# Optimization experiments

Measured on AMD Instinct MI355X. Metric: run time of the kernel, lower is better.

Reference implementation:

```python
import jax, jax.numpy as jnp
import numpy as np

D_MODEL = 1024
N_HEADS = 16
D_FF = 4096
EPS = 1e-6


def _linear_params(key, d_in, d_out):
    kw, kb = jax.random.split(key)
    bound = 1.0 / np.sqrt(d_in)
    W = jax.random.uniform(kw, (d_out, d_in), minval=-bound, maxval=bound, dtype=jnp.float32)
    b = jax.random.uniform(kb, (d_out,), minval=-bound, maxval=bound, dtype=jnp.float32)
    return W, b


def setup_inputs() -> dict:
    key = jax.random.key(0)
    keys = jax.random.split(key, 8)
    x = jax.random.normal(keys[0], (4, 2048, D_MODEL), dtype=jnp.float32)
    mask = jnp.ones((4, 1, 1, 2048), dtype=jnp.bool_)
    Wq, bq = _linear_params(keys[1], D_MODEL, D_MODEL)
    Wk, bk = _linear_params(keys[2], D_MODEL, D_MODEL)
    Wv, bv = _linear_params(keys[3], D_MODEL, D_MODEL)
    Wo, bo = _linear_params(keys[4], D_MODEL, D_MODEL)
    W1, b1 = _linear_params(keys[5], D_MODEL, D_FF)
    W2, b2 = _linear_params(keys[6], D_FF, D_MODEL)
    ln1_g = jnp.ones((D_MODEL,), jnp.float32); ln1_b = jnp.zeros((D_MODEL,), jnp.float32)
    ln2_g = jnp.ones((D_MODEL,), jnp.float32); ln2_b = jnp.zeros((D_MODEL,), jnp.float32)
    return {"x": x, "mask": mask,
            "Wq": Wq, "bq": bq, "Wk": Wk, "bk": bk, "Wv": Wv, "bv": bv,
            "Wo": Wo, "bo": bo, "W1": W1, "b1": b1, "W2": W2, "b2": b2,
            "ln1_g": ln1_g, "ln1_b": ln1_b, "ln2_g": ln2_g, "ln2_b": ln2_b}


def _layernorm(x, g, b):
    # torch LayerNorm here uses unbiased std and divides by (std + eps)
    mean = jnp.mean(x, axis=-1, keepdims=True)
    std = jnp.std(x, axis=-1, keepdims=True, ddof=1)
    return g * (x - mean) / (std + EPS) + b


def _gelu_tanh(x):
    c = np.sqrt(2.0 / np.pi).astype(np.float32)
    return 0.5 * x * (1.0 + jnp.tanh(c * (x + 0.044715 * x * x * x)))


def _mha(xn, mask, Wq, bq, Wk, bk, Wv, bv, Wo, bo):
    B, S, D = xn.shape
    d_k = D // N_HEADS
    def proj(W, b):
        y = jnp.einsum('bsd,ed->bse', xn, W) + b
        return y.reshape(B, S, N_HEADS, d_k).transpose(0, 2, 1, 3)  # [B,h,S,d_k]
    q, k, v = proj(Wq, bq), proj(Wk, bk), proj(Wv, bv)
    scores = jnp.einsum('bhqd,bhkd->bhqk', q, k) / np.float32(np.sqrt(d_k))
    scores = jnp.where(mask, scores, jnp.float32(-1e9))
    p = jax.nn.softmax(scores, axis=-1)
    o = jnp.einsum('bhqk,bhkd->bhqd', p, v)
    o = o.transpose(0, 2, 1, 3).reshape(B, S, D)
    return jnp.einsum('bsd,ed->bse', o, Wo) + bo


def reference(x, mask, Wq, bq, Wk, bk, Wv, bv, Wo, bo, W1, b1, W2, b2,
              ln1_g, ln1_b, ln2_g, ln2_b):
    xn = _layernorm(x, ln1_g, ln1_b)
    y = x + _mha(xn, mask, Wq, bq, Wk, bk, Wv, bv, Wo, bo)
    yn = _layernorm(y, ln2_g, ln2_b)
    h = _gelu_tanh(jnp.einsum('bsd,fd->bsf', yn, W1) + b1)
    z = y + (jnp.einsum('bsf,df->bsd', h, W2) + b2)
    return z
```

## Files before the change

### kernel.cpp

```cpp
#include <hip/hip_runtime.h>

typedef __bf16 bf16;
typedef __bf16 bfx4 __attribute__((ext_vector_type(4)));
typedef __bf16 bfx8 __attribute__((ext_vector_type(8)));
typedef float  fx4  __attribute__((ext_vector_type(4)));

#define NTOK 8192
#define DM   1024
#define DFF  4096
#define SEQ  2048
#define NH   16
#define DK   64

#define OFF_WQKV 0ull
#define OFF_WO   (OFF_WQKV + 3072ull*1024*2)
#define OFF_W1   (OFF_WO   + 1024ull*1024*2)
#define OFF_W2   (OFF_W1   + 4096ull*1024*2)
#define OFF_BQKV (OFF_W2   + 4096ull*1024*2)
#define OFF_XN   (OFF_BQKV + 3072ull*4)
#define OFF_QKV  (OFF_XN   + 8192ull*1024*2)
#define OFF_ATTN (OFF_QKV  + 8192ull*3072*2)
#define OFF_Y    (OFF_ATTN + 8192ull*1024*2)
#define OFF_VT   OFF_Y
#define OFF_H    OFF_XN
#define OFF_YN   OFF_ATTN

__device__ __forceinline__ void gload16(const void* g, void* l) {
  __builtin_amdgcn_global_load_lds(
      (__attribute__((address_space(1))) void*)(g),
      (__attribute__((address_space(3))) void*)(l), 16, 0, 0);
}

__device__ __forceinline__ float gelu_tanh(float x) {
  float u = 0.7978845608028654f * (x + 0.044715f * x * x * x);
  float t = 1.f - 2.f / (__expf(2.f * u) + 1.f);
  return 0.5f * x * (1.f + t);
}

__global__ __launch_bounds__(256) void cast_all(const float* __restrict__ Wq,
                                                const float* __restrict__ Wk,
                                                const float* __restrict__ Wv,
                                                const float* __restrict__ Wo,
                                                const float* __restrict__ W1,
                                                const float* __restrict__ W2,
                                                bf16* __restrict__ dst) {
  const int bid = blockIdx.x;
  const int g = bid >> 9;
  const int j = ((bid & 511) << 11) + threadIdx.x * 8;
  const float* s;
  if (g == 0) s = Wq;
  else if (g == 1) s = Wk;
  else if (g == 2) s = Wv;
  else if (g == 3) s = Wo;
  else if (g < 8) s = W1 + (size_t)(g - 4) * 1048576;
  else s = W2 + (size_t)(g - 8) * 1048576;
  const float4 a = *(const float4*)(s + j);
  const float4 c = *(const float4*)(s + j + 4);
  bfx8 o;
  o[0] = (bf16)a.x; o[1] = (bf16)a.y; o[2] = (bf16)a.z; o[3] = (bf16)a.w;
  o[4] = (bf16)c.x; o[5] = (bf16)c.y; o[6] = (bf16)c.z; o[7] = (bf16)c.w;
  *(bfx8*)(dst + (size_t)g * 1048576 + j) = o;
}

__global__ void biask(const float* __restrict__ bq, const float* __restrict__ bk,
                      const float* __restrict__ bv, float* __restrict__ o) {
  const int i = blockIdx.x * 1024 + threadIdx.x;
  const float* s = blockIdx.x == 0 ? bq : (blockIdx.x == 1 ? bk : bv);
  o[i] = s[threadIdx.x];
}

__global__ __launch_bounds__(256) void ln_kernel(const float* __restrict__ x,
                                                 const float* __restrict__ g,
                                                 const float* __restrict__ b,
                                                 bf16* __restrict__ out) {
  const int row = blockIdx.x;
  const int c = threadIdx.x * 4;
  const float4 v = *(const float4*)&x[(size_t)row * DM + c];
  float s1 = v.x + v.y + v.z + v.w;
  float s2 = v.x * v.x + v.y * v.y + v.z * v.z + v.w * v.w;
  #pragma unroll
  for (int o = 32; o; o >>= 1) { s1 += __shfl_xor(s1, o); s2 += __shfl_xor(s2, o); }
  __shared__ float red[8];
  const int wid = threadIdx.x >> 6;
  if ((threadIdx.x & 63) == 0) { red[wid] = s1; red[4 + wid] = s2; }
  __syncthreads();
  s1 = red[0] + red[1] + red[2] + red[3];
  s2 = red[4] + red[5] + red[6] + red[7];
  const float mean = s1 * (1.f / (float)DM);
  const float var = (s2 - (float)DM * mean * mean) * (1.f / (float)(DM - 1));
  const float inv = 1.f / (sqrtf(fmaxf(var, 0.f)) + 1e-6f);
  bfx4 o;
  o[0] = (bf16)(g[c + 0] * (v.x - mean) * inv + b[c + 0]);
  o[1] = (bf16)(g[c + 1] * (v.y - mean) * inv + b[c + 1]);
  o[2] = (bf16)(g[c + 2] * (v.z - mean) * inv + b[c + 2]);
  o[3] = (bf16)(g[c + 3] * (v.w - mean) * inv + b[c + 3]);
  *(bfx4*)&out[(size_t)row * DM + c] = o;
}

template <int EPI, int VSPLIT>
__global__ __launch_bounds__(256) void gemmdp(const bf16* __restrict__ A,
                                              const bf16* __restrict__ B,
                                              const float* __restrict__ bias,
                                              const float* __restrict__ resid,
                                              bf16* __restrict__ vt,
                                              void* __restrict__ outp,
                                              int M, int N, int K) {
  __shared__ char lds[65536];
  const int tid = threadIdx.x;
  const int lane = tid & 63, w = tid >> 6;
  const int l15 = lane & 15, lhi = lane >> 4;
  const int wm = w >> 1, wn = w & 1;

  const int nwg = gridDim.x * gridDim.y;
  int bid = blockIdx.y * gridDim.x + blockIdx.x;
  bid = (bid & 7) * (nwg >> 3) + (bid >> 3);
  const int m0 = (bid % gridDim.x) * 128;
  const int n0 = (bid / gridDim.x) * 128;
  const size_t str = (size_t)K * 2;

  const int r_s = tid >> 3;
  const int c2  = (tid & 7) * 16;
  const int csw = c2 ^ ((r_s & 7) << 4);
  const char* ap = (const char*)A + (size_t)(m0 + r_s) * str + csw;
  const char* bp = (const char*)B + (size_t)(n0 + r_s) * str + csw;

  auto stage = [&](int buf) {
    char* dst = lds + buf * 32768 + tid * 16;
    #pragma unroll
    for (int s = 0; s < 4; ++s)
      gload16(ap + (size_t)(s * 32) * str, dst + s * 4096);
    #pragma unroll
    for (int s = 0; s < 4; ++s)
      gload16(bp + (size_t)(s * 32) * str, dst + 16384 + s * 4096);
    ap += 128; bp += 128;
  };

  fx4 acc[4][4] = {};
  const int asw = (l15 & 7) << 4;
  const int nK = K >> 6;

  stage(0);

  #pragma unroll 1
  for (int t = 0; t < nK; ++t) {
    asm volatile("s_waitcnt vmcnt(0)" ::: "memory");
    __builtin_amdgcn_s_barrier();
    asm volatile("" ::: "memory");
    if (t + 1 < nK) stage((t + 1) & 1);

    const char* Ab = lds + (t & 1) * 32768;
    const char* Bb = Ab + 16384;
    #pragma unroll
    for (int kk = 0; kk < 2; ++kk) {
      bfx8 af[4], bv[4];
      #pragma unroll
      for (int i = 0; i < 4; ++i)
        af[i] = *(const bfx8*)(Ab + (wm * 64 + i * 16 + l15) * 128 +
                               ((kk * 64 + lhi * 16) ^ asw));
      #pragma unroll
      for (int j = 0; j < 4; ++j)
        bv[j] = *(const bfx8*)(Bb + (wn * 64 + j * 16 + l15) * 128 +
                               ((kk * 64 + lhi * 16) ^ asw));
      __builtin_amdgcn_s_setprio(1);
      #pragma unroll
      for (int i = 0; i < 4; ++i)
        #pragma unroll
        for (int j = 0; j < 4; ++j)
          acc[i][j] = __builtin_amdgcn_mfma_f32_16x16x32_bf16(af[i], bv[j], acc[i][j], 0, 0, 0);
      __builtin_amdgcn_s_setprio(0);
    }
  }

  const int rb = m0 + wm * 64 + lhi * 4;
  const int cb = n0 + wn * 64 + l15;
  #pragma unroll
  for (int j = 0; j < 4; ++j) {
    const int c = cb + j * 16;
    const float bv = bias[c];
    if (VSPLIT && c >= 2048) {
      const int hd = c - 2048;
      #pragma unroll
      for (int i = 0; i < 4; ++i) {
        const int tok = rb + i * 16;
        const int bb = tok >> 11;
        bfx4 o4;
        #pragma unroll
        for (int e = 0; e < 4; ++e) o4[e] = (bf16)(acc[i][j][e] + bv);
        *(bfx4*)&vt[((size_t)(bb * 1024 + hd)) * SEQ + (tok & 2047)] = o4;
      }
    } else {
      #pragma unroll
      for (int i = 0; i < 4; ++i) {
        #pragma unroll
        for (int e = 0; e < 4; ++e) {
          const size_t idx = (size_t)(rb + i * 16 + e) * N + c;
          float v = acc[i][j][e] + bv;
          if constexpr (EPI == 1) v = gelu_tanh(v);
          if constexpr (EPI == 2) {
            ((float*)outp)[idx] = v + resid[idx];
          } else {
            ((bf16*)outp)[idx] = (bf16)v;
          }
        }
      }
    }
  }
}

__global__ __launch_bounds__(256, 4) void attn_kernel(const bf16* __restrict__ QKV,
                                                      const bf16* __restrict__ VT,
                                                      bf16* __restrict__ O) {
  __shared__ bf16 lds[2][2][4096];
  const int tid = threadIdx.x;
  const int lane = tid & 63, w = tid >> 6;
  const int l15 = lane & 15, lhi = lane >> 4;
  int id = blockIdx.x;
  id = (id & 7) * 128 + (id >> 3);
  const int q0 = (id & 15) * 128;
  const int h = (id >> 4) & 15;
  const int b = id >> 8;
  const size_t tokbase = (size_t)b * SEQ;

  const int lin0 = w * 1024 + lane * 16;
  const int lin1 = lin0 + 4096;
  const int row0 = lin0 >> 7, row1 = lin1 >> 7;
  const int cs0 = (lin0 & 127) ^ ((row0 & 7) << 4);
  const int cs1 = (lin1 & 127) ^ ((row1 & 7) << 4);
  const char* kp0 = (const char*)QKV + ((tokbase + row0) * 3072 + 1024 + h * 64) * 2 + cs0;
  const char* kp1 = (const char*)QKV + ((tokbase + row1) * 3072 + 1024 + h * 64) * 2 + cs1;
  const char* vbase = (const char*)(VT + (size_t)((b * NH + h) * 64) * SEQ);
  const char* vp0 = vbase + (size_t)row0 * (SEQ * 2) + cs0;
  const char* vp1 = vbase + (size_t)row1 * (SEQ * 2) + cs1;
  char* const ldsb = (char*)&lds[0][0][0];
  int dofs = 0;
  const long KADV = 64l * 3072 * 2;
  const long VADV = 64l * 2;

  auto stage = [&]() {
    gload16(kp0, ldsb + dofs + lin0);
    gload16(kp1, ldsb + dofs + lin1);
    gload16(vp0, ldsb + dofs + 8192 + lin0);
    gload16(vp1, ldsb + dofs + 8192 + lin1);
    kp0 += KADV; kp1 += KADV; vp0 += VADV; vp1 += VADV;
    dofs ^= 16384;
  };

  stage();

  bfx8 qf[2][2];
  #pragma unroll
  for (int m = 0; m < 2; ++m)
    #pragma unroll
    for (int kk = 0; kk < 2; ++kk) {
      bfx8 raw = *(const bfx8*)&QKV[(tokbase + q0 + w * 32 + m * 16 + l15) * 3072
                                    + h * DK + kk * 32 + lhi * 8];
      bfx8 sc;
      #pragma unroll
      for (int e = 0; e < 8; ++e) sc[e] = (bf16)((float)raw[e] * 0.18033688011112042f);
      qf[m][kk] = sc;
    }

  fx4 acc[2][4] = {};
  fx4 lsum[2] = {};
  bfx8 ones;
  #pragma unroll
  for (int e = 0; e < 8; ++e) ones[e] = (bf16)1.0f;

  const int NT = SEQ / 64;
  #pragma unroll 2
  for (int t = 0; t < NT; ++t) {
    if (t + 1 < NT) {
      stage();
      asm volatile("s_waitcnt vmcnt(4)" ::: "memory");
    } else {
      asm volatile("s_waitcnt vmcnt(0)" ::: "memory");
    }
    __builtin_amdgcn_s_barrier();

    const char* Kl = ldsb + ((t & 1) << 14);
    const char* Vl = Kl + 8192;

    fx4 s[2][4] = {};
    #pragma unroll
    for (int kk = 0; kk < 2; ++kk) {
      bfx8 kf[4];
      #pragma unroll
      for (int n = 0; n < 4; ++n) {
        const int row = n * 16 + l15;
        kf[n] = *(const bfx8*)(Kl + row * 128 + ((kk * 64 + lhi * 16) ^ ((row & 7) << 4)));
      }
      __builtin_amdgcn_s_setprio(1);
      #pragma unroll
      for (int m = 0; m < 2; ++m)
        #pragma unroll
        for (int n = 0; n < 4; ++n)
          s[m][n] = __builtin_amdgcn_mfma_f32_16x16x32_bf16(kf[n], qf[m][kk], s[m][n], 0, 0, 0);
      __builtin_amdgcn_s_setprio(0);
    }

    uint32_t pu[2][4][2];
    #pragma unroll
    for (int m = 0; m < 2; ++m)
      #pragma unroll
      for (int n = 0; n < 4; ++n) {
        const float p0 = exp2f(s[m][n][0]);
        const float p1 = exp2f(s[m][n][1]);
        const float p2 = exp2f(s[m][n][2]);
        const float p3 = exp2f(s[m][n][3]);
        union { bf16 h2[2]; uint32_t u; } c0, c1;
        c0.h2[0] = (bf16)p0; c0.h2[1] = (bf16)p1;
        c1.h2[0] = (bf16)p2; c1.h2[1] = (bf16)p3;
        pu[m][n][0] = c0.u; pu[m][n][1] = c1.u;
      }

    #pragma unroll
    for (int kk = 0; kk < 2; ++kk) {
      bfx8 pB[2];
      #pragma unroll
      for (int m = 0; m < 2; ++m) {
        union { uint32_t u[4]; bfx8 v; } cb2;
        cb2.u[0] = pu[m][2 * kk][0];
        cb2.u[1] = pu[m][2 * kk][1];
        cb2.u[2] = pu[m][2 * kk + 1][0];
        cb2.u[3] = pu[m][2 * kk + 1][1];
        pB[m] = cb2.v;
      }
      __builtin_amdgcn_s_setprio(1);
      #pragma unroll
      for (int m = 0; m < 2; ++m)
        lsum[m] = __builtin_amdgcn_mfma_f32_16x16x32_bf16(ones, pB[m], lsum[m], 0, 0, 0);
      __builtin_amdgcn_s_setprio(0);
      #pragma unroll
      for (int dn = 0; dn < 4; ++dn) {
        const int row = dn * 16 + l15;
        const int sw = (row & 7) << 4;
        union { bfx4 q2[2]; bfx8 v; } vv;
        vv.q2[0] = *(const bfx4*)(Vl + row * 128 + ((kk * 64 + lhi * 8) ^ sw));
        vv.q2[1] = *(const bfx4*)(Vl + row * 128 + ((kk * 64 + 32 + lhi * 8) ^ sw));
        __builtin_amdgcn_s_setprio(1);
        #pragma unroll
        for (int m = 0; m < 2; ++m)
          acc[m][dn] = __builtin_amdgcn_mfma_f32_16x16x32_bf16(vv.v, pB[m], acc[m][dn], 0, 0, 0);
        __builtin_amdgcn_s_setprio(0);
      }
    }

    asm volatile("s_waitcnt lgkmcnt(0)" ::: "memory");
    __builtin_amdgcn_s_barrier();
  }

  __syncthreads();
  bf16* Ep = &lds[0][0][0] + w * 2048;
  const float rinv0 = __builtin_amdgcn_rcpf(lsum[0][0]);
  const float rinv1 = __builtin_amdgcn_rcpf(lsum[1][0]);
  #pragma unroll
  for (int m = 0; m < 2; ++m) {
    const int qr = m * 16 + l15;
    const int sw = (qr & 7) << 4;
    const float ri = m ? rinv1 : rinv0;
    #pragma unroll
    for (int dn = 0; dn < 4; ++dn)
      #pragma unroll
      for (int e = 0; e < 4; ++e) {
        const int d = dn * 16 + lhi * 4 + e;
        *(bf16*)((char*)Ep + qr * 128 + ((2 * d) ^ sw)) = (bf16)(acc[m][dn][e] * ri);
      }
  }
  __syncthreads();
  #pragma unroll
  for (int j = 0; j < 4; ++j) {
    const int qr = lane >> 1;
    const int cbyte = (lane & 1) * 64 + j * 16;
    bfx8 v = *(const bfx8*)((char*)Ep + qr * 128 + (cbyte ^ ((qr & 7) << 4)));
    *(bfx8*)&O[(tokbase + q0 + w * 32 + qr) * (size_t)DM + h * DK + (lane & 1) * 32 + j * 8] = v;
  }
}

extern "C" void kernel_launch(void* const* d_in, const int* in_sizes, int n_in,
                              void* d_out, int out_size, void* d_ws, size_t ws_size,
                              hipStream_t stream) {
  const float* x  = (const float*)d_in[0];
  const float* Wq = (const float*)d_in[2];
  const float* bq = (const float*)d_in[3];
  const float* Wk = (const float*)d_in[4];
  const float* bk = (const float*)d_in[5];
  const float* Wv = (const float*)d_in[6];
  const float* bv = (const float*)d_in[7];
  const float* Wo = (const float*)d_in[8];
  const float* bo = (const float*)d_in[9];
  const float* W1 = (const float*)d_in[10];
  const float* b1 = (const float*)d_in[11];
  const float* W2 = (const float*)d_in[12];
  const float* b2 = (const float*)d_in[13];
  const float* g1 = (const float*)d_in[14];
  const float* be1 = (const float*)d_in[15];
  const float* g2 = (const float*)d_in[16];
  const float* be2 = (const float*)d_in[17];

  char* ws = (char*)d_ws;
  bf16* WQKVb = (bf16*)(ws + OFF_WQKV);
  bf16* WOb   = (bf16*)(ws + OFF_WO);
  bf16* W1b   = (bf16*)(ws + OFF_W1);
  bf16* W2b   = (bf16*)(ws + OFF_W2);
  float* BQKV = (float*)(ws + OFF_BQKV);
  bf16* XN    = (bf16*)(ws + OFF_XN);
  bf16* QKVb  = (bf16*)(ws + OFF_QKV);
  bf16* ATTNb = (bf16*)(ws + OFF_ATTN);
  float* Yb   = (float*)(ws + OFF_Y);
  bf16* VTb   = (bf16*)(ws + OFF_VT);
  bf16* Hb    = (bf16*)(ws + OFF_H);
  bf16* YNb   = (bf16*)(ws + OFF_YN);

  cast_all<<<6144, 256, 0, stream>>>(Wq, Wk, Wv, Wo, W1, W2, WQKVb);
  biask<<<3, 1024, 0, stream>>>(bq, bk, bv, BQKV);

  ln_kernel<<<NTOK, 256, 0, stream>>>(x, g1, be1, XN);
  gemmdp<0, 1><<<dim3(64, 24), 256, 0, stream>>>(XN, WQKVb, BQKV, nullptr,
                                                 VTb, QKVb, NTOK, 3072, 1024);
  attn_kernel<<<1024, 256, 0, stream>>>(QKVb, VTb, ATTNb);
  gemmdp<2, 0><<<dim3(64, 8), 256, 0, stream>>>(ATTNb, WOb, bo, x, nullptr,
                                                Yb, NTOK, 1024, 1024);
  ln_kernel<<<NTOK, 256, 0, stream>>>(Yb, g2, be2, YNb);
  gemmdp<1, 0><<<dim3(64, 32), 256, 0, stream>>>(YNb, W1b, b1, nullptr,
                                                 nullptr, Hb, NTOK, 4096, 1024);
  gemmdp<2, 0><<<dim3(64, 8), 256, 0, stream>>>(Hb, W2b, b2, Yb, nullptr,
                                                (float*)d_out, NTOK, 1024, 4096);
}
```

Before: 442.2 us.

## Use 256x128 GEMM tiles with triple-buffered K=32 LDS pipeline

Replaces the 128x128 double-buffered GEMM with a 256x128 tile. It uses K-steps of 32, a 3-stage LDS ring (72KB of dynamic shared memory) and two-ahead prefetch with partial vmcnt waits. The block remap now walks m-major, and each wave holds 8x4 accumulators. The aim is more operand reuse per load and better overlap of global loads with MFMA. The cost is higher register pressure, one block per CU-slot pair, and a barrier every 32-wide K step.

```diff
diff --git a/kernel.cpp b/kernel.cpp
--- a/kernel.cpp
+++ b/kernel.cpp
@@ -98,103 +98,105 @@
 }
 
 template <int EPI, int VSPLIT>
-__global__ __launch_bounds__(256) void gemmdp(const bf16* __restrict__ A,
-                                              const bf16* __restrict__ B,
-                                              const float* __restrict__ bias,
-                                              const float* __restrict__ resid,
-                                              bf16* __restrict__ vt,
-                                              void* __restrict__ outp,
-                                              int M, int N, int K) {
-  __shared__ char lds[65536];
+__global__ __launch_bounds__(256, 2) void gemmk(const bf16* __restrict__ A,
+                                                const bf16* __restrict__ B,
+                                                const float* __restrict__ bias,
+                                                const float* __restrict__ resid,
+                                                bf16* __restrict__ vt,
+                                                void* __restrict__ outp,
+                                                int M, int N, int K) {
+  extern __shared__ char lds[];
   const int tid = threadIdx.x;
   const int lane = tid & 63, w = tid >> 6;
   const int l15 = lane & 15, lhi = lane >> 4;
   const int wm = w >> 1, wn = w & 1;
 
-  const int nwg = gridDim.x * gridDim.y;
-  int bid = blockIdx.y * gridDim.x + blockIdx.x;
-  bid = (bid & 7) * (nwg >> 3) + (bid >> 3);
-  const int m0 = (bid % gridDim.x) * 128;
-  const int n0 = (bid / gridDim.x) * 128;
+  const int gy = gridDim.y;
+  const int nwg = gridDim.x * gy;
+  const int L = blockIdx.y * gridDim.x + blockIdx.x;
+  const int wid = (L & 7) * (nwg >> 3) + (L >> 3);
+  const int m0 = (wid / gy) * 256;
+  const int n0 = (wid % gy) * 128;
   const size_t str = (size_t)K * 2;
 
-  const int r_s = tid >> 3;
-  const int c2  = (tid & 7) * 16;
-  const int csw = c2 ^ ((r_s & 7) << 4);
-  const char* ap = (const char*)A + (size_t)(m0 + r_s) * str + csw;
-  const char* bp = (const char*)B + (size_t)(n0 + r_s) * str + csw;
-
-  auto stage = [&](int buf) {
-    char* dst = lds + buf * 32768 + tid * 16;
-    #pragma unroll
-    for (int s = 0; s < 4; ++s)
-      gload16(ap + (size_t)(s * 32) * str, dst + s * 4096);
-    #pragma unroll
-    for (int s = 0; s < 4; ++s)
-      gload16(bp + (size_t)(s * 32) * str, dst + 16384 + s * 4096);
-    ap += 128; bp += 128;
+  const int rT = tid >> 2;
+  const int cT = ((tid & 3) ^ ((tid >> 3) & 3)) * 16;
+  const char* aS = (const char*)A + (size_t)(m0 + rT) * str + cT;
+  const char* bS = (const char*)B + (size_t)(n0 + rT) * str + cT;
+
+  auto stage = [&](int buf, int kt) {
+    const size_t kb = (size_t)kt * 64;
+    char* d = lds + buf * 24576 + tid * 16;
+    #pragma unroll
+    for (int p = 0; p < 4; ++p)
+      gload16(aS + (size_t)(p * 64) * str + kb, d + p * 4096);
+    #pragma unroll
+    for (int p = 0; p < 2; ++p)
+      gload16(bS + (size_t)(p * 64) * str + kb, d + 16384 + p * 4096);
   };
 
-  fx4 acc[4][4] = {};
-  const int asw = (l15 & 7) << 4;
-  const int nK = K >> 6;
-
-  stage(0);
+  fx4 acc[8][4] = {};
+  const int nK = K >> 5;
+
+  stage(0, 0);
+  stage(1, 1);
 
   #pragma unroll 1
   for (int t = 0; t < nK; ++t) {
-    asm volatile("s_waitcnt vmcnt(0)" ::: "memory");
+    if (t < nK - 1)
+      asm volatile("s_waitcnt vmcnt(6) lgkmcnt(0)" ::: "memory");
+    else
+      asm volatile("s_waitcnt vmcnt(0) lgkmcnt(0)" ::: "memory");
     __builtin_amdgcn_s_barrier();
     asm volatile("" ::: "memory");
-    if (t + 1 < nK) stage((t + 1) & 1);
-
-    const char* Ab = lds + (t & 1) * 32768;
+    if (t + 2 < nK) stage((t + 2) % 3, t + 2);
+
+    const char* Ab = lds + (t % 3) * 24576;
     const char* Bb = Ab + 16384;
-    #pragma unroll
-    for (int kk = 0; kk < 2; ++kk) {
-      bfx8 af[4], bv[4];
-      #pragma unroll
-      for (int i = 0; i < 4; ++i)
-        af[i] = *(const bfx8*)(Ab + (wm * 64 + i * 16 + l15) * 128 +
-                               ((kk * 64 + lhi * 16) ^ asw));
+    bfx8 af[8], bv[4];
+    #pragma unroll
+    for (int i = 0; i < 8; ++i) {
+      const int r = wm * 128 + i * 16 + l15;
+      af[i] = *(const bfx8*)(Ab + r * 64 + ((lhi * 16) ^ (((r >> 1) & 3) << 4)));
+    }
+    #pragma unroll
+    for (int j = 0; j < 4; ++j) {
+      const int r = wn * 64 + j * 16 + l15;
+      bv[j] = *(const bfx8*)(Bb + r * 64 + ((lhi * 16) ^ (((r >> 1) & 3) << 4)));
+    }
+    __builtin_amdgcn_s_setprio(1);
+    #pragma unroll
+    for (int i = 0; i < 8; ++i)
       #pragma unroll
       for (int j = 0; j < 4; ++j)
-        bv[j] = *(const bfx8*)(Bb + (wn * 64 + j * 16 + l15) * 128 +
-                               ((kk * 64 + lhi * 16) ^ asw));
-      __builtin_amdgcn_s_setprio(1);
-      #pragma unroll
-      for (int i = 0; i < 4; ++i)
-        #pragma unroll
-        for (int j = 0; j < 4; ++j)
-          acc[i][j] = __builtin_amdgcn_mfma_f32_16x16x32_bf16(af[i], bv[j], acc[i][j], 0, 0, 0);
-      __builtin_amdgcn_s_setprio(0);
-    }
+        acc[i][j] = __builtin_amdgcn_mfma_f32_16x16x32_bf16(af[i], bv[j], acc[i][j], 0, 0, 0);
+    __builtin_amdgcn_s_setprio(0);
   }
 
-  const int rb = m0 + wm * 64 + lhi * 4;
+  const int rb = m0 + wm * 128 + lhi * 4;
   const int cb = n0 + wn * 64 + l15;
   #pragma unroll
   for (int j = 0; j < 4; ++j) {
     const int c = cb + j * 16;
-    const float bv = bias[c];
+    const float bvv = bias[c];
     if (VSPLIT && c >= 2048) {
       const int hd = c - 2048;
       #pragma unroll
-      for (int i = 0; i < 4; ++i) {
+      for (int i = 0; i < 8; ++i) {
         const int tok = rb + i * 16;
         const int bb = tok >> 11;
         bfx4 o4;
         #pragma unroll
-        for (int e = 0; e < 4; ++e) o4[e] = (bf16)(acc[i][j][e] + bv);
+        for (int e = 0; e < 4; ++e) o4[e] = (bf16)(acc[i][j][e] + bvv);
         *(bfx4*)&vt[((size_t)(bb * 1024 + hd)) * SEQ + (tok & 2047)] = o4;
       }
     } else {
       #pragma unroll
-      for (int i = 0; i < 4; ++i) {
+      for (int i = 0; i < 8; ++i) {
         #pragma unroll
         for (int e = 0; e < 4; ++e) {
           const size_t idx = (size_t)(rb + i * 16 + e) * N + c;
-          float v = acc[i][j][e] + bv;
+          float v = acc[i][j][e] + bvv;
           if constexpr (EPI == 1) v = gelu_tanh(v);
           if constexpr (EPI == 2) {
             ((float*)outp)[idx] = v + resid[idx];
@@ -411,18 +413,25 @@
   bf16* Hb    = (bf16*)(ws + OFF_H);
   bf16* YNb   = (bf16*)(ws + OFF_YN);
 
+  hipFuncSetAttribute((const void*)&gemmk<0, 1>,
+                      hipFuncAttributeMaxDynamicSharedMemorySize, 73728);
+  hipFuncSetAttribute((const void*)&gemmk<1, 0>,
+                      hipFuncAttributeMaxDynamicSharedMemorySize, 73728);
+  hipFuncSetAttribute((const void*)&gemmk<2, 0>,
+                      hipFuncAttributeMaxDynamicSharedMemorySize, 73728);
+
   cast_all<<<6144, 256, 0, stream>>>(Wq, Wk, Wv, Wo, W1, W2, WQKVb);
   biask<<<3, 1024, 0, stream>>>(bq, bk, bv, BQKV);
 
   ln_kernel<<<NTOK, 256, 0, stream>>>(x, g1, be1, XN);
-  gemmdp<0, 1><<<dim3(64, 24), 256, 0, stream>>>(XN, WQKVb, BQKV, nullptr,
-                                                 VTb, QKVb, NTOK, 3072, 1024);
+  gemmk<0, 1><<<dim3(32, 24), 256, 73728, stream>>>(XN, WQKVb, BQKV, nullptr,
+                                                    VTb, QKVb, NTOK, 3072, 1024);
   attn_kernel<<<1024, 256, 0, stream>>>(QKVb, VTb, ATTNb);
-  gemmdp<2, 0><<<dim3(64, 8), 256, 0, stream>>>(ATTNb, WOb, bo, x, nullptr,
-                                                Yb, NTOK, 1024, 1024);
+  gemmk<2, 0><<<dim3(32, 8), 256, 73728, stream>>>(ATTNb, WOb, bo, x, nullptr,
+                                                   Yb, NTOK, 1024, 1024);
   ln_kernel<<<NTOK, 256, 0, stream>>>(Yb, g2, be2, YNb);
-  gemmdp<1, 0><<<dim3(64, 32), 256, 0, stream>>>(YNb, W1b, b1, nullptr,
-                                                 nullptr, Hb, NTOK, 4096, 1024);
-  gemmdp<2, 0><<<dim3(64, 8), 256, 0, stream>>>(Hb, W2b, b2, Yb, nullptr,
-                                                (float*)d_out, NTOK, 1024, 4096);
-}
+  gemmk<1, 0><<<dim3(32, 32), 256, 73728, stream>>>(YNb, W1b, b1, nullptr,
+                                                    nullptr, Hb, NTOK, 4096, 1024);
+  gemmk<2, 0><<<dim3(32, 8), 256, 73728, stream>>>(Hb, W2b, b2, Yb, nullptr,
+                                                   (float*)d_out, NTOK, 1024, 4096);
+}
```

Result: no change. 440.1 us (-0.5%).
